# Performance work log

Measured on AMD Instinct MI355X. Metric: run time of the kernel, lower is better.

Reference implementation:

```python
import jax, jax.numpy as jnp
import numpy as np

N_NODES = 4096
N_GRAPHS = 32
N = N_NODES * N_GRAPHS          # 131072 total nodes
DEG = 32
E = N * DEG                      # 4194304 edges
IN_CH = 16
OUT_CH = 2
EPS_BN = 1e-5


def setup_inputs() -> dict:
    key = jax.random.key(0)
    ks = jax.random.split(key, 24)
    rn = lambda k, s, scale=0.1: (jax.random.normal(k, s, dtype=jnp.float32) * scale)
    return {
        "x": jax.random.normal(ks[0], (N, IN_CH), dtype=jnp.float32),
        "edge_index": jax.random.randint(ks[1], (2, E), 0, N),
        "edge_attr": jax.random.uniform(ks[2], (E, 3), dtype=jnp.float32),
        # GraphConv1: 16 -> 20  (lin_rel has bias, lin_root has no bias; PyG GraphConv)
        "W_rel1": rn(ks[3], (IN_CH, 20)), "b1": jnp.zeros((20,), jnp.float32), "W_root1": rn(ks[4], (IN_CH, 20)),
        # GraphConv2: 20 -> 20
        "W_rel2": rn(ks[5], (20, 20)), "b2": jnp.zeros((20,), jnp.float32), "W_root2": rn(ks[6], (20, 20)),
        # GraphConv3: 20 -> 1
        "W_rel3": rn(ks[7], (20, 1)), "b3": jnp.zeros((1,), jnp.float32), "W_root3": rn(ks[8], (20, 1)),
        # BatchNorm1d(num_nodes) affine params (channel dim = node index)
        "bn1_g": jnp.ones((N_NODES,), jnp.float32), "bn1_b": jnp.zeros((N_NODES,), jnp.float32),
        "bn2_g": jnp.ones((N_NODES,), jnp.float32), "bn2_b": jnp.zeros((N_NODES,), jnp.float32),
        # fc layers, stored [in, out]
        "fc1_W": rn(ks[9], (N_NODES, 50), 0.02), "fc1_b": jnp.zeros((50,), jnp.float32),
        "fc2_W": rn(ks[10], (50, OUT_CH)), "fc2_b": jnp.zeros((OUT_CH,), jnp.float32),
        "num_graphs": N_GRAPHS,
    }


def _graph_conv(x, src, dst, w, W_rel, b_rel, W_root):
    # PyG GraphConv: out_i = lin_root(x_i) + lin_rel( sum_{j->i} w_ji * x_j )
    msg = x[src] * w[:, None]                              # [E, F] gather + scale
    agg = jax.ops.segment_sum(msg, dst, num_segments=x.shape[0])  # scatter-add
    return agg @ W_rel + b_rel + x @ W_root


def _bn_nodes(h3, gamma, beta):
    # BatchNorm1d(num_nodes) in training mode: h3 is [B, num_nodes, F];
    # normalize per node-channel over (batch, feat), biased variance (torch training).
    mu = jnp.mean(h3, axis=(0, 2), keepdims=True)
    var = jnp.var(h3, axis=(0, 2), keepdims=True)
    hn = (h3 - mu) * jax.lax.rsqrt(var + EPS_BN)
    return hn * gamma[None, :, None] + beta[None, :, None]


def reference(x, edge_index, edge_attr,
              W_rel1, b1, W_root1, W_rel2, b2, W_root2, W_rel3, b3, W_root3,
              bn1_g, bn1_b, bn2_g, bn2_b, fc1_W, fc1_b, fc2_W, fc2_b, num_graphs):
    src, dst = edge_index[0], edge_index[1]
    w = edge_attr[:, 2]
    B = num_graphs

    h = _graph_conv(x, src, dst, w, W_rel1, b1, W_root1)
    h = jax.nn.leaky_relu(h)                                   # slope 0.01, matches torch default
    h = _bn_nodes(h.reshape(B, -1, h.shape[-1]), bn1_g, bn1_b).reshape(-1, h.shape[-1])

    h = _graph_conv(h, src, dst, w, W_rel2, b2, W_root2)
    h = jax.nn.leaky_relu(h)
    h = _bn_nodes(h.reshape(B, -1, h.shape[-1]), bn2_g, bn2_b).reshape(-1, h.shape[-1])

    h = _graph_conv(h, src, dst, w, W_rel3, b3, W_root3)
    h = jax.nn.leaky_relu(h)
    h = h.reshape(B, -1)                                        # [B, num_nodes]

    # per-graph normalization; note: divides by var (not std), var is unbiased (torch.var default)
    eps = 1e-10
    out = (h - jnp.mean(h, axis=1, keepdims=True)) / (jnp.var(h, axis=1, keepdims=True, ddof=1) + eps)
    out = jax.nn.leaky_relu(out @ fc1_W + fc1_b)
    # dropout omitted (eval-mode identity)
    out = out @ fc2_W + fc2_b
    return (out, h)
```

## Files before the change

### kernel.cpp

```cpp
#include <hip/hip_runtime.h>
#include <hip/hip_fp16.h>

#define N_NODES 4096
#define N_GRAPHS 32
#define NTOT (N_NODES * N_GRAPHS)
#define NE (NTOT * 32)
#define C1 16
#define C2 20
#define CAP 72

#define NBUCK 512
#define BSHIFT 8
#define BMASK 255
#define CAPB 8960
#define EPB1 8192

__device__ __forceinline__ float lrelu(float v) { return v > 0.f ? v : 0.01f * v; }

__device__ __forceinline__ unsigned pack_edge(int src, float w) {
    int k = __float2int_rn(w * 32768.f);
    if (k > 32767) k = 32767;
    return (unsigned)src | ((unsigned)k << 17);
}
__device__ __forceinline__ void unpack_edge(unsigned p, int& src, float& w) {
    src = (int)(p & 0x1FFFFu);
    w = (float)(p >> 17) * 3.0517578125e-5f;
}

__device__ __forceinline__ uint4 pack8h(const float* v) {
    union { uint4 u4; __half h[8]; } c;
#pragma unroll
    for (int q = 0; q < 8; q++) c.h[q] = __float2half(v[q]);
    return c.u4;
}
__device__ __forceinline__ uint2 pack4h(const float* v) {
    union { uint2 u2; __half h[4]; } c;
#pragma unroll
    for (int q = 0; q < 4; q++) c.h[q] = __float2half(v[q]);
    return c.u2;
}
__device__ __forceinline__ void fma8(uint4 u, float wv, float* acc) {
    union { uint4 u4; __half2 h2[4]; } c; c.u4 = u;
#pragma unroll
    for (int q = 0; q < 4; q++) {
        float2 f = __half22float2(c.h2[q]);
        acc[2 * q]     += f.x * wv;
        acc[2 * q + 1] += f.y * wv;
    }
}
__device__ __forceinline__ void fma4(uint2 u, float wv, float* acc) {
    union { uint2 u2; __half2 h2[2]; } c; c.u2 = u;
#pragma unroll
    for (int q = 0; q < 2; q++) {
        float2 f = __half22float2(c.h2[q]);
        acc[2 * q]     += f.x * wv;
        acc[2 * q + 1] += f.y * wv;
    }
}
__device__ __forceinline__ void unp8(uint4 u, float* v) {
    union { uint4 u4; __half2 h2[4]; } c; c.u4 = u;
#pragma unroll
    for (int q = 0; q < 4; q++) {
        float2 f = __half22float2(c.h2[q]);
        v[2 * q] = f.x; v[2 * q + 1] = f.y;
    }
}
__device__ __forceinline__ void unp4(uint2 u, float* v) {
    union { uint2 u2; __half2 h2[2]; } c; c.u2 = u;
#pragma unroll
    for (int q = 0; q < 2; q++) {
        float2 f = __half22float2(c.h2[q]);
        v[2 * q] = f.x; v[2 * q + 1] = f.y;
    }
}

__global__ __launch_bounds__(256) void k_part1(const int* __restrict__ ei,
                                               const float* __restrict__ ea,
                                               int* __restrict__ gcur,
                                               uint2* __restrict__ part) {
    __shared__ int hist[NBUCK];
    __shared__ int cur[NBUCK];
    int t = threadIdx.x;
    hist[t] = 0; hist[t + 256] = 0;
    __syncthreads();
    int base = blockIdx.x * EPB1;
#pragma unroll 4
    for (int i = 0; i < EPB1 / 256; i++) {
        int d = ei[NE + base + i * 256 + t];
        atomicAdd(&hist[d >> BSHIFT], 1);
    }
    __syncthreads();
    cur[t]       = atomicAdd(&gcur[t], hist[t]);
    cur[t + 256] = atomicAdd(&gcur[t + 256], hist[t + 256]);
    __syncthreads();
#pragma unroll 4
    for (int i = 0; i < EPB1 / 256; i++) {
        int e = base + i * 256 + t;
        int d = ei[NE + e];
        int b = d >> BSHIFT;
        int p = atomicAdd(&cur[b], 1);
        if (p < CAPB)
            part[(size_t)b * CAPB + p] = make_uint2(pack_edge(ei[e], ea[3 * e + 2]),
                                                    (unsigned)(d & BMASK));
    }
}

__global__ __launch_bounds__(256) void k_part2(const int* __restrict__ gcur,
                                               const uint2* __restrict__ part,
                                               unsigned* __restrict__ slots,
                                               int* __restrict__ cnt) {
    __shared__ int cur[256];
    int t = threadIdx.x;
    cur[t] = 0;
    __syncthreads();
    int b = blockIdx.x;
    int nrec = gcur[b]; if (nrec > CAPB) nrec = CAPB;
    const uint2* rp = part + (size_t)b * CAPB;
    int nb = b << BSHIFT;
    for (int i = t; i < nrec; i += 256) {
        uint2 r = rp[i];
        int ld = (int)r.y;
        int pos = atomicAdd(&cur[ld], 1);
        if (pos < CAP) slots[(size_t)pos * NTOT + nb + ld] = r.x;
    }
    __syncthreads();
    cnt[nb + t] = cur[t];
}

__global__ void k_fill_slots(const int* __restrict__ ei, const float* __restrict__ ea,
                             int* __restrict__ cnt, unsigned* __restrict__ slots) {
    int e = blockIdx.x * 256 + threadIdx.x;
    if (e >= NE) return;
    int d = ei[NE + e];
    int pos = atomicAdd(&cnt[d], 1);
    if (pos < CAP) slots[(size_t)pos * NTOT + d] = pack_edge(ei[e], ea[3 * e + 2]);
}

__global__ void k_xcast(const float* __restrict__ x, uint4* __restrict__ xa, uint4* __restrict__ xb) {
    int n = blockIdx.x * 256 + threadIdx.x;
    if (n >= NTOT) return;
    float xr[C1];
    const float4* xp = (const float4*)(x + (size_t)n * C1);
#pragma unroll
    for (int q = 0; q < 4; q++) ((float4*)xr)[q] = xp[q];
    xa[n] = pack8h(xr);
    xb[n] = pack8h(xr + 8);
}

__global__ __launch_bounds__(256) void k_conv1(const float* __restrict__ x,
                        const uint4* __restrict__ xa, const uint4* __restrict__ xb,
                        const unsigned* __restrict__ slots, const int* __restrict__ cnt,
                        const float* __restrict__ Wr, const float* __restrict__ bb,
                        const float* __restrict__ Wo, float* __restrict__ t1) {
    __shared__ float sWr[C1 * C2], sWo[C1 * C2], sb[C2];
    for (int k = threadIdx.x; k < C1 * C2; k += 256) { sWr[k] = Wr[k]; sWo[k] = Wo[k]; }
    if (threadIdx.x < C2) sb[threadIdx.x] = bb[threadIdx.x];
    __syncthreads();
    int n = blockIdx.x * 256 + threadIdx.x;
    int m = cnt[n]; if (m > CAP) m = CAP;
    float acc[C1];
#pragma unroll
    for (int i = 0; i < C1; i++) acc[i] = 0.f;
    {
        int i = 0;
        for (; i + 4 <= m; i += 4) {
            unsigned p0 = __builtin_nontemporal_load(slots + (size_t)(i + 0) * NTOT + n);
            unsigned p1 = __builtin_nontemporal_load(slots + (size_t)(i + 1) * NTOT + n);
            unsigned p2 = __builtin_nontemporal_load(slots + (size_t)(i + 2) * NTOT + n);
            unsigned p3 = __builtin_nontemporal_load(slots + (size_t)(i + 3) * NTOT + n);
            int s0, s1, s2, s3; float w0, w1, w2, w3;
            unpack_edge(p0, s0, w0); unpack_edge(p1, s1, w1);
            unpack_edge(p2, s2, w2); unpack_edge(p3, s3, w3);
            uint4 u0 = xa[s0], u1 = xa[s1], u2 = xa[s2], u3 = xa[s3];
            fma8(u0, w0, acc); fma8(u1, w1, acc); fma8(u2, w2, acc); fma8(u3, w3, acc);
        }
        for (; i < m; i++) {
            unsigned p = __builtin_nontemporal_load(slots + (size_t)i * NTOT + n);
            int s; float w; unpack_edge(p, s, w);
            fma8(xa[s], w, acc);
        }
    }
    {
        int i = 0;
        for (; i + 4 <= m; i += 4) {
            unsigned p0 = __builtin_nontemporal_load(slots + (size_t)(i + 0) * NTOT + n);
            unsigned p1 = __builtin_nontemporal_load(slots + (size_t)(i + 1) * NTOT + n);
            unsigned p2 = __builtin_nontemporal_load(slots + (size_t)(i + 2) * NTOT + n);
            unsigned p3 = __builtin_nontemporal_load(slots + (size_t)(i + 3) * NTOT + n);
            int s0, s1, s2, s3; float w0, w1, w2, w3;
            unpack_edge(p0, s0, w0); unpack_edge(p1, s1, w1);
            unpack_edge(p2, s2, w2); unpack_edge(p3, s3, w3);
            uint4 u0 = xb[s0], u1 = xb[s1], u2 = xb[s2], u3 = xb[s3];
            fma8(u0, w0, acc + 8); fma8(u1, w1, acc + 8); fma8(u2, w2, acc + 8); fma8(u3, w3, acc + 8);
        }
        for (; i < m; i++) {
            unsigned p = __builtin_nontemporal_load(slots + (size_t)i * NTOT + n);
            int s; float w; unpack_edge(p, s, w);
            fma8(xb[s], w, acc + 8);
        }
    }
    float xr[C1];
    const float4* xp = (const float4*)(x + (size_t)n * C1);
#pragma unroll
    for (int q = 0; q < 4; q++) ((float4*)xr)[q] = xp[q];
    float outv[C2];
#pragma unroll
    for (int j = 0; j < C2; j++) {
        float a = sb[j];
#pragma unroll
        for (int i = 0; i < C1; i++) a += acc[i] * sWr[i * C2 + j] + xr[i] * sWo[i * C2 + j];
        outv[j] = lrelu(a);
    }
    float4* op = (float4*)(t1 + (size_t)n * C2);
#pragma unroll
    for (int q = 0; q < 5; q++) op[q] = ((float4*)outv)[q];
}

__global__ void k_stats(const float* __restrict__ t, float* __restrict__ mu, float* __restrict__ rs) {
    int i = blockIdx.x;
    float s = 0.f, ss = 0.f;
    for (int k = threadIdx.x; k < N_GRAPHS * C2; k += 64) {
        int g = k / C2, j = k - g * C2;
        float v = t[((size_t)(g * N_NODES + i)) * C2 + j];
        s += v; ss += v * v;
    }
#pragma unroll
    for (int off = 32; off > 0; off >>= 1) { s += __shfl_down(s, off); ss += __shfl_down(ss, off); }
    if (threadIdx.x == 0) {
        float m = s * (1.f / (N_GRAPHS * C2));
        float var = ss * (1.f / (N_GRAPHS * C2)) - m * m;
        mu[i] = m;
        rs[i] = rsqrtf(var + 1e-5f);
    }
}

__global__ void k_bn_apply(const float* __restrict__ t, const float* __restrict__ mu,
                           const float* __restrict__ rs, const float* __restrict__ gam,
                           const float* __restrict__ bet, uint4* __restrict__ hnA,
                           uint2* __restrict__ hnB) {
    int n = blockIdx.x * 256 + threadIdx.x;
    if (n >= NTOT) return;
    int i = n & (N_NODES - 1);
    float sc = rs[i] * gam[i];
    float sh = bet[i] - mu[i] * sc;
    float v[C2];
    const float4* tp = (const float4*)(t + (size_t)n * C2);
#pragma unroll
    for (int q = 0; q < 5; q++) ((float4*)v)[q] = tp[q];
#pragma unroll
    for (int j = 0; j < C2; j++) v[j] = v[j] * sc + sh;
    hnA[n] = pack8h(v);
    uint2* hp = hnB + (size_t)n * 3;
    hp[0] = pack4h(v + 8);
    hp[1] = pack4h(v + 12);
    hp[2] = pack4h(v + 16);
}

__global__ __launch_bounds__(256) void k_conv2(const uint4* __restrict__ hnA,
                        const uint2* __restrict__ hnB,
                        const unsigned* __restrict__ slots, const int* __restrict__ cnt,
                        const float* __restrict__ Wr, const float* __restrict__ bb,
                        const float* __restrict__ Wo, float* __restrict__ t2) {
    __shared__ float sWr[C2 * C2], sWo[C2 * C2], sb[C2];
    for (int k = threadIdx.x; k < C2 * C2; k += 256) { sWr[k] = Wr[k]; sWo[k] = Wo[k]; }
    if (threadIdx.x < C2) sb[threadIdx.x] = bb[threadIdx.x];
    __syncthreads();
    int n = blockIdx.x * 256 + threadIdx.x;
    int m = cnt[n]; if (m > CAP) m = CAP;
    float acc[C2];
#pragma unroll
    for (int i = 0; i < C2; i++) acc[i] = 0.f;
    {
        int i = 0;
        for (; i + 4 <= m; i += 4) {
            unsigned p0 = __builtin_nontemporal_load(slots + (size_t)(i + 0) * NTOT + n);
            unsigned p1 = __builtin_nontemporal_load(slots + (size_t)(i + 1) * NTOT + n);
            unsigned p2 = __builtin_nontemporal_load(slots + (size_t)(i + 2) * NTOT + n);
            unsigned p3 = __builtin_nontemporal_load(slots + (size_t)(i + 3) * NTOT + n);
            int s0, s1, s2, s3; float w0, w1, w2, w3;
            unpack_edge(p0, s0, w0); unpack_edge(p1, s1, w1);
            unpack_edge(p2, s2, w2); unpack_edge(p3, s3, w3);
            uint4 u0 = hnA[s0], u1 = hnA[s1], u2 = hnA[s2], u3 = hnA[s3];
            fma8(u0, w0, acc); fma8(u1, w1, acc); fma8(u2, w2, acc); fma8(u3, w3, acc);
        }
        for (; i < m; i++) {
            unsigned p = __builtin_nontemporal_load(slots + (size_t)i * NTOT + n);
            int s; float w; unpack_edge(p, s, w);
            fma8(hnA[s], w, acc);
        }
    }
    {
        int i = 0;
        for (; i + 4 <= m; i += 4) {
            unsigned p0 = __builtin_nontemporal_load(slots + (size_t)(i + 0) * NTOT + n);
            unsigned p1 = __builtin_nontemporal_load(slots + (size_t)(i + 1) * NTOT + n);
            unsigned p2 = __builtin_nontemporal_load(slots + (size_t)(i + 2) * NTOT + n);
            unsigned p3 = __builtin_nontemporal_load(slots + (size_t)(i + 3) * NTOT + n);
            int s0, s1, s2, s3; float w0, w1, w2, w3;
            unpack_edge(p0, s0, w0); unpack_edge(p1, s1, w1);
            unpack_edge(p2, s2, w2); unpack_edge(p3, s3, w3);
            const uint2* r0 = hnB + (size_t)s0 * 3;
            const uint2* r1 = hnB + (size_t)s1 * 3;
            const uint2* r2 = hnB + (size_t)s2 * 3;
            const uint2* r3 = hnB + (size_t)s3 * 3;
            uint2 a0 = r0[0], b0 = r0[1], c0 = r0[2];
            uint2 a1 = r1[0], b1 = r1[1], c1 = r1[2];
            uint2 a2 = r2[0], b2 = r2[1], c2 = r2[2];
            uint2 a3 = r3[0], b3 = r3[1], c3 = r3[2];
            fma4(a0, w0, acc + 8); fma4(b0, w0, acc + 12); fma4(c0, w0, acc + 16);
            fma4(a1, w1, acc + 8); fma4(b1, w1, acc + 12); fma4(c1, w1, acc + 16);
            fma4(a2, w2, acc + 8); fma4(b2, w2, acc + 12); fma4(c2, w2, acc + 16);
            fma4(a3, w3, acc + 8); fma4(b3, w3, acc + 12); fma4(c3, w3, acc + 16);
        }
        for (; i < m; i++) {
            unsigned p = __builtin_nontemporal_load(slots + (size_t)i * NTOT + n);
            int s; float w; unpack_edge(p, s, w);
            const uint2* r = hnB + (size_t)s * 3;
            fma4(r[0], w, acc + 8); fma4(r[1], w, acc + 12); fma4(r[2], w, acc + 16);
        }
    }
    float h[C2];
    unp8(hnA[n], h);
    {
        const uint2* r = hnB + (size_t)n * 3;
        unp4(r[0], h + 8); unp4(r[1], h + 12); unp4(r[2], h + 16);
    }
    float outv[C2];
#pragma unroll
    for (int j = 0; j < C2; j++) {
        float a = sb[j];
#pragma unroll
        for (int i = 0; i < C2; i++) a += acc[i] * sWr[i * C2 + j] + h[i] * sWo[i * C2 + j];
        outv[j] = lrelu(a);
    }
    float4* op = (float4*)(t2 + (size_t)n * C2);
#pragma unroll
    for (int q = 0; q < 5; q++) op[q] = ((float4*)outv)[q];
}

__global__ void k_bn2_proj(const float* __restrict__ t, const float* __restrict__ mu,
                           const float* __restrict__ rs, const float* __restrict__ gam,
                           const float* __restrict__ bet, const float* __restrict__ Wr3,
                           const float* __restrict__ b3, const float* __restrict__ Wo3,
                           float* __restrict__ y, float* __restrict__ r2) {
    __shared__ float sWr[C2], sWo[C2];
    if (threadIdx.x < C2) { sWr[threadIdx.x] = Wr3[threadIdx.x]; sWo[threadIdx.x] = Wo3[threadIdx.x]; }
    __syncthreads();
    int n = blockIdx.x * 256 + threadIdx.x;
    if (n >= NTOT) return;
    int i = n & (N_NODES - 1);
    float sc = rs[i] * gam[i];
    float sh = bet[i] - mu[i] * sc;
    float v[C2];
    const float4* tp = (const float4*)(t + (size_t)n * C2);
#pragma unroll
    for (int q = 0; q < 5; q++) ((float4*)v)[q] = tp[q];
    float ay = 0.f, ar = 0.f;
#pragma unroll
    for (int j = 0; j < C2; j++) {
        float hv = v[j] * sc + sh;
        ay += hv * sWr[j];
        ar += hv * sWo[j];
    }
    y[n] = ay;
    r2[n] = ar + b3[0];
}

__global__ __launch_bounds__(256) void k_conv3(const float* __restrict__ y, const float* __restrict__ r2,
                        const unsigned* __restrict__ slots, const int* __restrict__ cnt,
                        float* __restrict__ hout, float* __restrict__ gsum, float* __restrict__ gss) {
    __shared__ float ls[4], lss[4];
    int n = blockIdx.x * 256 + threadIdx.x;
    int m = cnt[n]; if (m > CAP) m = CAP;
    float a = 0.f;
    int i = 0;
    for (; i + 4 <= m; i += 4) {
        unsigned p0 = __builtin_nontemporal_load(slots + (size_t)(i + 0) * NTOT + n);
        unsigned p1 = __builtin_nontemporal_load(slots + (size_t)(i + 1) * NTOT + n);
        unsigned p2 = __builtin_nontemporal_load(slots + (size_t)(i + 2) * NTOT + n);
        unsigned p3 = __builtin_nontemporal_load(slots + (size_t)(i + 3) * NTOT + n);
        int s0, s1, s2, s3; float w0, w1, w2, w3;
        unpack_edge(p0, s0, w0); unpack_edge(p1, s1, w1);
        unpack_edge(p2, s2, w2); unpack_edge(p3, s3, w3);
        a += y[s0] * w0 + y[s1] * w1 + y[s2] * w2 + y[s3] * w3;
    }
    for (; i < m; i++) {
        unsigned p = __builtin_nontemporal_load(slots + (size_t)i * NTOT + n);
        int s; float w; unpack_edge(p, s, w);
        a += y[s] * w;
    }
    float v = lrelu(a + r2[n]);
    hout[n] = v;
    float s = v, ss = v * v;
#pragma unroll
    for (int o = 32; o > 0; o >>= 1) { s += __shfl_down(s, o); ss += __shfl_down(ss, o); }
    int wid = threadIdx.x >> 6, lid = threadIdx.x & 63;
    if (lid == 0) { ls[wid] = s; lss[wid] = ss; }
    __syncthreads();
    if (threadIdx.x == 0) {
        int g = blockIdx.x >> 4;
        atomicAdd(&gsum[g], ls[0] + ls[1] + ls[2] + ls[3]);
        atomicAdd(&gss[g], lss[0] + lss[1] + lss[2] + lss[3]);
    }
}

__global__ void k_fc1(const float* __restrict__ h, const float* __restrict__ gsum,
                      const float* __restrict__ gss, const float* __restrict__ W,
                      const float* __restrict__ b, float* __restrict__ z) {
    __shared__ float ls[4];
    int blk = blockIdx.x;
    int g = blk / 50, k = blk - g * 50;
    float mu = gsum[g] / N_NODES;
    float var = (gss[g] - N_NODES * mu * mu) / (N_NODES - 1);
    float inv = 1.f / (var + 1e-10f);
    const float* hr = h + (size_t)g * N_NODES;
    float p = 0.f;
    for (int n = threadIdx.x; n < N_NODES; n += 256)
        p += (hr[n] - mu) * inv * W[(size_t)n * 50 + k];
#pragma unroll
    for (int off = 32; off > 0; off >>= 1) p += __shfl_down(p, off);
    int wid = threadIdx.x >> 6, lid = threadIdx.x & 63;
    if (lid == 0) ls[wid] = p;
    __syncthreads();
    if (threadIdx.x == 0) {
        float S = ls[0] + ls[1] + ls[2] + ls[3];
        z[g * 50 + k] = lrelu(S + b[k]);
    }
}

__global__ void k_fc2(const float* __restrict__ z, const float* __restrict__ W,
                      const float* __restrict__ b, float* __restrict__ out) {
    int t = threadIdx.x;
    if (t >= N_GRAPHS * 2) return;
    int g = t >> 1, o = t & 1;
    float acc = b[o];
#pragma unroll
    for (int k = 0; k < 50; k++) acc += z[g * 50 + k] * W[k * 2 + o];
    out[g * 2 + o] = acc;
}

extern "C" void kernel_launch(void* const* d_in, const int* in_sizes, int n_in,
                              void* d_out, int out_size, void* d_ws, size_t ws_size,
                              hipStream_t stream) {
    const float* x    = (const float*)d_in[0];
    const int*   ei   = (const int*)d_in[1];
    const float* ea   = (const float*)d_in[2];
    const float* Wr1  = (const float*)d_in[3];
    const float* b1   = (const float*)d_in[4];
    const float* Wo1  = (const float*)d_in[5];
    const float* Wr2  = (const float*)d_in[6];
    const float* b2   = (const float*)d_in[7];
    const float* Wo2  = (const float*)d_in[8];
    const float* Wr3  = (const float*)d_in[9];
    const float* b3   = (const float*)d_in[10];
    const float* Wo3  = (const float*)d_in[11];
    const float* bn1g = (const float*)d_in[12];
    const float* bn1b = (const float*)d_in[13];
    const float* bn2g = (const float*)d_in[14];
    const float* bn2b = (const float*)d_in[15];
    const float* fc1W = (const float*)d_in[16];
    const float* fc1b = (const float*)d_in[17];
    const float* fc2W = (const float*)d_in[18];
    const float* fc2b = (const float*)d_in[19];
    float* out = (float*)d_out;

    const size_t part_bytes  = (size_t)NBUCK * CAPB * sizeof(uint2);
    const size_t slots_bytes = (size_t)NTOT * CAP * sizeof(unsigned);
    const size_t tail_bytes  = (size_t)NTOT * C2 * sizeof(float)
                             + (size_t)NTOT * 16 * 3
                             + (size_t)NTOT * 24
                             + (size_t)NTOT * 2 * sizeof(float)
                             + (size_t)NTOT * sizeof(int)
                             + (size_t)(NBUCK + 4 * N_NODES + 8 * N_GRAPHS + N_GRAPHS * 50 + 64) * sizeof(float);
    const bool useSort = ws_size >= part_bytes + slots_bytes + tail_bytes;

    char* wsb = (char*)d_ws;
    uint2*    part  = (uint2*)wsb;     wsb += useSort ? part_bytes : 0;
    unsigned* slots = (unsigned*)wsb;  wsb += slots_bytes;
    float*    bufA  = (float*)wsb;     wsb += (size_t)NTOT * C2 * sizeof(float);
    uint4*    xa    = (uint4*)wsb;     wsb += (size_t)NTOT * 16;
    uint4*    xb    = (uint4*)wsb;     wsb += (size_t)NTOT * 16;
    uint4*    hnA   = (uint4*)wsb;     wsb += (size_t)NTOT * 16;
    uint2*    hnB   = (uint2*)wsb;     wsb += (size_t)NTOT * 24;
    float*    yv    = (float*)wsb;     wsb += (size_t)NTOT * sizeof(float);
    float*    r2v   = (float*)wsb;     wsb += (size_t)NTOT * sizeof(float);
    int*      cnt   = (int*)wsb;       wsb += (size_t)NTOT * sizeof(int);
    int*      gcur  = (int*)wsb;       wsb += NBUCK * sizeof(int);
    float*    mu1   = (float*)wsb;     wsb += N_NODES * sizeof(float);
    float*    rs1   = (float*)wsb;     wsb += N_NODES * sizeof(float);
    float*    mu2   = (float*)wsb;     wsb += N_NODES * sizeof(float);
    float*    rs2   = (float*)wsb;     wsb += N_NODES * sizeof(float);
    float*    gsum  = (float*)wsb;     wsb += N_GRAPHS * sizeof(float);
    float*    gss   = (float*)wsb;     wsb += N_GRAPHS * sizeof(float);
    float*    z     = (float*)wsb;     wsb += N_GRAPHS * 50 * sizeof(float);

    const int EB = (NE + 255) / 256;
    const int NB = (NTOT + 255) / 256;

    hipMemsetAsync(gsum, 0, 2 * N_GRAPHS * sizeof(float), stream);
    k_xcast<<<NB, 256, 0, stream>>>(x, xa, xb);
    if (useSort) {
        hipMemsetAsync(gcur, 0, NBUCK * sizeof(int), stream);
        k_part1<<<NE / EPB1, 256, 0, stream>>>(ei, ea, gcur, part);
        k_part2<<<NBUCK, 256, 0, stream>>>(gcur, part, slots, cnt);
    } else {
        hipMemsetAsync(cnt, 0, (size_t)NTOT * sizeof(int), stream);
        k_fill_slots<<<EB, 256, 0, stream>>>(ei, ea, cnt, slots);
    }

    k_conv1<<<NB, 256, 0, stream>>>(x, xa, xb, slots, cnt, Wr1, b1, Wo1, bufA);
    k_stats<<<N_NODES, 64, 0, stream>>>(bufA, mu1, rs1);
    k_bn_apply<<<NB, 256, 0, stream>>>(bufA, mu1, rs1, bn1g, bn1b, hnA, hnB);

    k_conv2<<<NB, 256, 0, stream>>>(hnA, hnB, slots, cnt, Wr2, b2, Wo2, bufA);
    k_stats<<<N_NODES, 64, 0, stream>>>(bufA, mu2, rs2);
    k_bn2_proj<<<NB, 256, 0, stream>>>(bufA, mu2, rs2, bn2g, bn2b, Wr3, b3, Wo3, yv, r2v);

    k_conv3<<<NB, 256, 0, stream>>>(yv, r2v, slots, cnt, out + 64, gsum, gss);

    k_fc1<<<N_GRAPHS * 50, 256, 0, stream>>>(out + 64, gsum, gss, fc1W, fc1b, z);
    k_fc2<<<1, 64, 0, stream>>>(z, fc2W, fc2b, out);
}
```

Before: 457.3 us.

## Split conv edge loops across wavefronts and stage partition writes in LDS

The three graph-conv kernels now assign several threads per node: the edge list is split in halves and the feature channels in groups across wavefronts, and partial sums are combined through shared memory before the dense projection, which is itself spread over four threads per node. This raises parallelism and memory-level concurrency for the gather-heavy aggregation, at the cost of extra LDS traffic, a barrier, and redundant slot loads. The bucket partition kernel now sorts records locally in LDS by bucket with a prefix scan and writes them out contiguously, so global writes coalesce instead of scattering per atomic slot. conv1 also reads root features from the fp16 copies rather than the fp32 input, which changes precision slightly.

```diff
diff --git a/kernel.cpp b/kernel.cpp
--- a/kernel.cpp
+++ b/kernel.cpp
@@ -78,30 +78,55 @@
                                                const float* __restrict__ ea,
                                                int* __restrict__ gcur,
                                                uint2* __restrict__ part) {
-    __shared__ int hist[NBUCK];
-    __shared__ int cur[NBUCK];
+    __shared__ unsigned lrecA[EPB1];
+    __shared__ unsigned char lrecB[EPB1];
+    __shared__ int hist[NBUCK], sscan[NBUCK], base[NBUCK], lcur[NBUCK];
+    __shared__ int ts[256];
     int t = threadIdx.x;
     hist[t] = 0; hist[t + 256] = 0;
     __syncthreads();
-    int base = blockIdx.x * EPB1;
-#pragma unroll 4
+    int eb = blockIdx.x * EPB1;
+    int dreg[EPB1 / 256];
+#pragma unroll
     for (int i = 0; i < EPB1 / 256; i++) {
-        int d = ei[NE + base + i * 256 + t];
+        int d = ei[NE + eb + i * 256 + t];
+        dreg[i] = d;
         atomicAdd(&hist[d >> BSHIFT], 1);
     }
     __syncthreads();
-    cur[t]       = atomicAdd(&gcur[t], hist[t]);
-    cur[t + 256] = atomicAdd(&gcur[t + 256], hist[t + 256]);
-    __syncthreads();
-#pragma unroll 4
+    int a0 = hist[2 * t], a1 = hist[2 * t + 1];
+    ts[t] = a0 + a1;
+    __syncthreads();
+    for (int d = 1; d < 256; d <<= 1) {
+        int v = (t >= d) ? ts[t - d] : 0;
+        __syncthreads();
+        ts[t] += v;
+        __syncthreads();
+    }
+    int excl = (t == 0) ? 0 : ts[t - 1];
+    sscan[2 * t] = excl;
+    sscan[2 * t + 1] = excl + a0;
+    lcur[2 * t] = excl;
+    lcur[2 * t + 1] = excl + a0;
+    base[t]       = atomicAdd(&gcur[t], hist[t]);
+    base[t + 256] = atomicAdd(&gcur[t + 256], hist[t + 256]);
+    __syncthreads();
+#pragma unroll
     for (int i = 0; i < EPB1 / 256; i++) {
-        int e = base + i * 256 + t;
-        int d = ei[NE + e];
+        int e = eb + i * 256 + t;
+        int d = dreg[i];
         int b = d >> BSHIFT;
-        int p = atomicAdd(&cur[b], 1);
-        if (p < CAPB)
-            part[(size_t)b * CAPB + p] = make_uint2(pack_edge(ei[e], ea[3 * e + 2]),
-                                                    (unsigned)(d & BMASK));
+        int pos = atomicAdd(&lcur[b], 1);
+        lrecA[pos] = pack_edge(ei[e], ea[3 * e + 2]);
+        lrecB[pos] = (unsigned char)(d & BMASK);
+    }
+    __syncthreads();
+    for (int j = t; j < EPB1; j += 256) {
+        int lo = 0, hi = NBUCK - 1;
+        while (lo < hi) { int mid = (lo + hi + 1) >> 1; if (sscan[mid] <= j) lo = mid; else hi = mid - 1; }
+        int b = lo;
+        int dp = base[b] + (j - sscan[b]);
+        if (dp < CAPB) part[(size_t)b * CAPB + dp] = make_uint2(lrecA[j], (unsigned)lrecB[j]);
     }
 }
 
@@ -147,73 +172,65 @@
     xb[n] = pack8h(xr + 8);
 }
 
-__global__ __launch_bounds__(256) void k_conv1(const float* __restrict__ x,
-                        const uint4* __restrict__ xa, const uint4* __restrict__ xb,
+__global__ __launch_bounds__(256) void k_conv1(const uint4* __restrict__ xa, const uint4* __restrict__ xb,
                         const unsigned* __restrict__ slots, const int* __restrict__ cnt,
                         const float* __restrict__ Wr, const float* __restrict__ bb,
                         const float* __restrict__ Wo, float* __restrict__ t1) {
     __shared__ float sWr[C1 * C2], sWo[C1 * C2], sb[C2];
+    __shared__ float sacc[4][64][8];
     for (int k = threadIdx.x; k < C1 * C2; k += 256) { sWr[k] = Wr[k]; sWo[k] = Wo[k]; }
     if (threadIdx.x < C2) sb[threadIdx.x] = bb[threadIdx.x];
-    __syncthreads();
-    int n = blockIdx.x * 256 + threadIdx.x;
-    int m = cnt[n]; if (m > CAP) m = CAP;
-    float acc[C1];
-#pragma unroll
-    for (int i = 0; i < C1; i++) acc[i] = 0.f;
-    {
-        int i = 0;
-        for (; i + 4 <= m; i += 4) {
-            unsigned p0 = __builtin_nontemporal_load(slots + (size_t)(i + 0) * NTOT + n);
-            unsigned p1 = __builtin_nontemporal_load(slots + (size_t)(i + 1) * NTOT + n);
-            unsigned p2 = __builtin_nontemporal_load(slots + (size_t)(i + 2) * NTOT + n);
-            unsigned p3 = __builtin_nontemporal_load(slots + (size_t)(i + 3) * NTOT + n);
-            int s0, s1, s2, s3; float w0, w1, w2, w3;
-            unpack_edge(p0, s0, w0); unpack_edge(p1, s1, w1);
-            unpack_edge(p2, s2, w2); unpack_edge(p3, s3, w3);
-            uint4 u0 = xa[s0], u1 = xa[s1], u2 = xa[s2], u3 = xa[s3];
-            fma8(u0, w0, acc); fma8(u1, w1, acc); fma8(u2, w2, acc); fma8(u3, w3, acc);
-        }
-        for (; i < m; i++) {
-            unsigned p = __builtin_nontemporal_load(slots + (size_t)i * NTOT + n);
-            int s; float w; unpack_edge(p, s, w);
-            fma8(xa[s], w, acc);
-        }
-    }
-    {
-        int i = 0;
-        for (; i + 4 <= m; i += 4) {
-            unsigned p0 = __builtin_nontemporal_load(slots + (size_t)(i + 0) * NTOT + n);
-            unsigned p1 = __builtin_nontemporal_load(slots + (size_t)(i + 1) * NTOT + n);
-            unsigned p2 = __builtin_nontemporal_load(slots + (size_t)(i + 2) * NTOT + n);
-            unsigned p3 = __builtin_nontemporal_load(slots + (size_t)(i + 3) * NTOT + n);
-            int s0, s1, s2, s3; float w0, w1, w2, w3;
-            unpack_edge(p0, s0, w0); unpack_edge(p1, s1, w1);
-            unpack_edge(p2, s2, w2); unpack_edge(p3, s3, w3);
-            uint4 u0 = xb[s0], u1 = xb[s1], u2 = xb[s2], u3 = xb[s3];
-            fma8(u0, w0, acc + 8); fma8(u1, w1, acc + 8); fma8(u2, w2, acc + 8); fma8(u3, w3, acc + 8);
-        }
-        for (; i < m; i++) {
-            unsigned p = __builtin_nontemporal_load(slots + (size_t)i * NTOT + n);
-            int s; float w; unpack_edge(p, s, w);
-            fma8(xb[s], w, acc + 8);
-        }
-    }
+    int nl = threadIdx.x & 63;
+    int sub = threadIdx.x >> 6;
+    int gn = blockIdx.x * 64 + nl;
+    int m = cnt[gn]; if (m > CAP) m = CAP;
+    int h0 = m >> 1;
+    int lo = (sub & 1) ? h0 : 0;
+    int hi = (sub & 1) ? m : h0;
+    const uint4* va = (sub < 2) ? xa : xb;
+    float acc[8];
+#pragma unroll
+    for (int q = 0; q < 8; q++) acc[q] = 0.f;
+    int i = lo;
+    for (; i + 4 <= hi; i += 4) {
+        unsigned p0 = __builtin_nontemporal_load(slots + (size_t)(i + 0) * NTOT + gn);
+        unsigned p1 = __builtin_nontemporal_load(slots + (size_t)(i + 1) * NTOT + gn);
+        unsigned p2 = __builtin_nontemporal_load(slots + (size_t)(i + 2) * NTOT + gn);
+        unsigned p3 = __builtin_nontemporal_load(slots + (size_t)(i + 3) * NTOT + gn);
+        int s0, s1, s2, s3; float w0, w1, w2, w3;
+        unpack_edge(p0, s0, w0); unpack_edge(p1, s1, w1);
+        unpack_edge(p2, s2, w2); unpack_edge(p3, s3, w3);
+        uint4 u0 = va[s0], u1 = va[s1], u2 = va[s2], u3 = va[s3];
+        fma8(u0, w0, acc); fma8(u1, w1, acc); fma8(u2, w2, acc); fma8(u3, w3, acc);
+    }
+    for (; i < hi; i++) {
+        unsigned p = __builtin_nontemporal_load(slots + (size_t)i * NTOT + gn);
+        int s; float w; unpack_edge(p, s, w);
+        fma8(va[s], w, acc);
+    }
+#pragma unroll
+    for (int q = 0; q < 8; q++) sacc[sub][nl][q] = acc[q];
+    __syncthreads();
+    int n2 = threadIdx.x >> 2, qq = threadIdx.x & 3;
+    int gn2 = blockIdx.x * 64 + n2;
+    float accf[C1];
+#pragma unroll
+    for (int q = 0; q < 8; q++) accf[q] = sacc[0][n2][q] + sacc[1][n2][q];
+#pragma unroll
+    for (int q = 0; q < 8; q++) accf[8 + q] = sacc[2][n2][q] + sacc[3][n2][q];
     float xr[C1];
-    const float4* xp = (const float4*)(x + (size_t)n * C1);
-#pragma unroll
-    for (int q = 0; q < 4; q++) ((float4*)xr)[q] = xp[q];
-    float outv[C2];
-#pragma unroll
-    for (int j = 0; j < C2; j++) {
+    unp8(xa[gn2], xr); unp8(xb[gn2], xr + 8);
+    float outv[5];
+#pragma unroll
+    for (int jj = 0; jj < 5; jj++) {
+        int j = qq * 5 + jj;
         float a = sb[j];
 #pragma unroll
-        for (int i = 0; i < C1; i++) a += acc[i] * sWr[i * C2 + j] + xr[i] * sWo[i * C2 + j];
-        outv[j] = lrelu(a);
-    }
-    float4* op = (float4*)(t1 + (size_t)n * C2);
-#pragma unroll
-    for (int q = 0; q < 5; q++) op[q] = ((float4*)outv)[q];
+        for (int q = 0; q < C1; q++) a += accf[q] * sWr[q * C2 + j] + xr[q] * sWo[q * C2 + j];
+        outv[jj] = lrelu(a);
+    }
+#pragma unroll
+    for (int jj = 0; jj < 5; jj++) t1[(size_t)gn2 * C2 + qq * 5 + jj] = outv[jj];
 }
 
 __global__ void k_stats(const float* __restrict__ t, float* __restrict__ mu, float* __restrict__ rs) {
@@ -262,40 +279,50 @@
                         const float* __restrict__ Wr, const float* __restrict__ bb,
                         const float* __restrict__ Wo, float* __restrict__ t2) {
     __shared__ float sWr[C2 * C2], sWo[C2 * C2], sb[C2];
+    __shared__ float saccA[2][64][8];
+    __shared__ float saccB[2][64][12];
     for (int k = threadIdx.x; k < C2 * C2; k += 256) { sWr[k] = Wr[k]; sWo[k] = Wo[k]; }
     if (threadIdx.x < C2) sb[threadIdx.x] = bb[threadIdx.x];
-    __syncthreads();
-    int n = blockIdx.x * 256 + threadIdx.x;
-    int m = cnt[n]; if (m > CAP) m = CAP;
-    float acc[C2];
-#pragma unroll
-    for (int i = 0; i < C2; i++) acc[i] = 0.f;
-    {
-        int i = 0;
-        for (; i + 4 <= m; i += 4) {
-            unsigned p0 = __builtin_nontemporal_load(slots + (size_t)(i + 0) * NTOT + n);
-            unsigned p1 = __builtin_nontemporal_load(slots + (size_t)(i + 1) * NTOT + n);
-            unsigned p2 = __builtin_nontemporal_load(slots + (size_t)(i + 2) * NTOT + n);
-            unsigned p3 = __builtin_nontemporal_load(slots + (size_t)(i + 3) * NTOT + n);
+    int nl = threadIdx.x & 63;
+    int sub = threadIdx.x >> 6;
+    int gn = blockIdx.x * 64 + nl;
+    int m = cnt[gn]; if (m > CAP) m = CAP;
+    int h0 = m >> 1;
+    int lo = (sub & 1) ? h0 : 0;
+    int hi = (sub & 1) ? m : h0;
+    if (sub < 2) {
+        float acc[8];
+#pragma unroll
+        for (int q = 0; q < 8; q++) acc[q] = 0.f;
+        int i = lo;
+        for (; i + 4 <= hi; i += 4) {
+            unsigned p0 = __builtin_nontemporal_load(slots + (size_t)(i + 0) * NTOT + gn);
+            unsigned p1 = __builtin_nontemporal_load(slots + (size_t)(i + 1) * NTOT + gn);
+            unsigned p2 = __builtin_nontemporal_load(slots + (size_t)(i + 2) * NTOT + gn);
+            unsigned p3 = __builtin_nontemporal_load(slots + (size_t)(i + 3) * NTOT + gn);
             int s0, s1, s2, s3; float w0, w1, w2, w3;
             unpack_edge(p0, s0, w0); unpack_edge(p1, s1, w1);
             unpack_edge(p2, s2, w2); unpack_edge(p3, s3, w3);
             uint4 u0 = hnA[s0], u1 = hnA[s1], u2 = hnA[s2], u3 = hnA[s3];
             fma8(u0, w0, acc); fma8(u1, w1, acc); fma8(u2, w2, acc); fma8(u3, w3, acc);
         }
-        for (; i < m; i++) {
-            unsigned p = __builtin_nontemporal_load(slots + (size_t)i * NTOT + n);
+        for (; i < hi; i++) {
+            unsigned p = __builtin_nontemporal_load(slots + (size_t)i * NTOT + gn);
             int s; float w; unpack_edge(p, s, w);
             fma8(hnA[s], w, acc);
         }
-    }
-    {
-        int i = 0;
-        for (; i + 4 <= m; i += 4) {
-            unsigned p0 = __builtin_nontemporal_load(slots + (size_t)(i + 0) * NTOT + n);
-            unsigned p1 = __builtin_nontemporal_load(slots + (size_t)(i + 1) * NTOT + n);
-            unsigned p2 = __builtin_nontemporal_load(slots + (size_t)(i + 2) * NTOT + n);
-            unsigned p3 = __builtin_nontemporal_load(slots + (size_t)(i + 3) * NTOT + n);
+#pragma unroll
+        for (int q = 0; q < 8; q++) saccA[sub][nl][q] = acc[q];
+    } else {
+        float acc[12];
+#pragma unroll
+        for (int q = 0; q < 12; q++) acc[q] = 0.f;
+        int i = lo;
+        for (; i + 4 <= hi; i += 4) {
+            unsigned p0 = __builtin_nontemporal_load(slots + (size_t)(i + 0) * NTOT + gn);
+            unsigned p1 = __builtin_nontemporal_load(slots + (size_t)(i + 1) * NTOT + gn);
+            unsigned p2 = __builtin_nontemporal_load(slots + (size_t)(i + 2) * NTOT + gn);
+            unsigned p3 = __builtin_nontemporal_load(slots + (size_t)(i + 3) * NTOT + gn);
             int s0, s1, s2, s3; float w0, w1, w2, w3;
             unpack_edge(p0, s0, w0); unpack_edge(p1, s1, w1);
             unpack_edge(p2, s2, w2); unpack_edge(p3, s3, w3);
@@ -307,35 +334,45 @@
             uint2 a1 = r1[0], b1 = r1[1], c1 = r1[2];
             uint2 a2 = r2[0], b2 = r2[1], c2 = r2[2];
             uint2 a3 = r3[0], b3 = r3[1], c3 = r3[2];
-            fma4(a0, w0, acc + 8); fma4(b0, w0, acc + 12); fma4(c0, w0, acc + 16);
-            fma4(a1, w1, acc + 8); fma4(b1, w1, acc + 12); fma4(c1, w1, acc + 16);
-            fma4(a2, w2, acc + 8); fma4(b2, w2, acc + 12); fma4(c2, w2, acc + 16);
-            fma4(a3, w3, acc + 8); fma4(b3, w3, acc + 12); fma4(c3, w3, acc + 16);
+            fma4(a0, w0, acc); fma4(b0, w0, acc + 4); fma4(c0, w0, acc + 8);
+            fma4(a1, w1, acc); fma4(b1, w1, acc + 4); fma4(c1, w1, acc + 8);
+            fma4(a2, w2, acc); fma4(b2, w2, acc + 4); fma4(c2, w2, acc + 8);
+            fma4(a3, w3, acc); fma4(b3, w3, acc + 4); fma4(c3, w3, acc + 8);
         }
-        for (; i < m; i++) {
-            unsigned p = __builtin_nontemporal_load(slots + (size_t)i * NTOT + n);
+        for (; i < hi; i++) {
+            unsigned p = __builtin_nontemporal_load(slots + (size_t)i * NTOT + gn);
             int s; float w; unpack_edge(p, s, w);
             const uint2* r = hnB + (size_t)s * 3;
-            fma4(r[0], w, acc + 8); fma4(r[1], w, acc + 12); fma4(r[2], w, acc + 16);
+            fma4(r[0], w, acc); fma4(r[1], w, acc + 4); fma4(r[2], w, acc + 8);
         }
-    }
+#pragma unroll
+        for (int q = 0; q < 12; q++) saccB[sub - 2][nl][q] = acc[q];
+    }
+    __syncthreads();
+    int n2 = threadIdx.x >> 2, qq = threadIdx.x & 3;
+    int gn2 = blockIdx.x * 64 + n2;
+    float accf[C2];
+#pragma unroll
+    for (int q = 0; q < 8; q++) accf[q] = saccA[0][n2][q] + saccA[1][n2][q];
+#pragma unroll
+    for (int q = 0; q < 12; q++) accf[8 + q] = saccB[0][n2][q] + saccB[1][n2][q];
     float h[C2];
-    unp8(hnA[n], h);
+    unp8(hnA[gn2], h);
     {
-        const uint2* r = hnB + (size_t)n * 3;
+        const uint2* r = hnB + (size_t)gn2 * 3;
         unp4(r[0], h + 8); unp4(r[1], h + 12); unp4(r[2], h + 16);
     }
-    float outv[C2];
-#pragma unroll
-    for (int j = 0; j < C2; j++) {
+    float outv[5];
+#pragma unroll
+    for (int jj = 0; jj < 5; jj++) {
+        int j = qq * 5 + jj;
         float a = sb[j];
 #pragma unroll
-        for (int i = 0; i < C2; i++) a += acc[i] * sWr[i * C2 + j] + h[i] * sWo[i * C2 + j];
-        outv[j] = lrelu(a);
-    }
-    float4* op = (float4*)(t2 + (size_t)n * C2);
-#pragma unroll
-    for (int q = 0; q < 5; q++) op[q] = ((float4*)outv)[q];
+        for (int q = 0; q < C2; q++) a += accf[q] * sWr[q * C2 + j] + h[q] * sWo[q * C2 + j];
+        outv[jj] = lrelu(a);
+    }
+#pragma unroll
+    for (int jj = 0; jj < 5; jj++) t2[(size_t)gn2 * C2 + qq * 5 + jj] = outv[jj];
 }
 
 __global__ void k_bn2_proj(const float* __restrict__ t, const float* __restrict__ mu,
@@ -369,12 +406,18 @@
 __global__ __launch_bounds__(256) void k_conv3(const float* __restrict__ y, const float* __restrict__ r2,
                         const unsigned* __restrict__ slots, const int* __restrict__ cnt,
                         float* __restrict__ hout, float* __restrict__ gsum, float* __restrict__ gss) {
+    __shared__ float pbuf[2][128];
     __shared__ float ls[4], lss[4];
-    int n = blockIdx.x * 256 + threadIdx.x;
+    int nl = threadIdx.x & 127;
+    int half = threadIdx.x >> 7;
+    int n = blockIdx.x * 128 + nl;
     int m = cnt[n]; if (m > CAP) m = CAP;
+    int h0 = m >> 1;
+    int lo = half ? h0 : 0;
+    int hi = half ? m : h0;
     float a = 0.f;
-    int i = 0;
-    for (; i + 4 <= m; i += 4) {
+    int i = lo;
+    for (; i + 4 <= hi; i += 4) {
         unsigned p0 = __builtin_nontemporal_load(slots + (size_t)(i + 0) * NTOT + n);
         unsigned p1 = __builtin_nontemporal_load(slots + (size_t)(i + 1) * NTOT + n);
         unsigned p2 = __builtin_nontemporal_load(slots + (size_t)(i + 2) * NTOT + n);
@@ -384,13 +427,18 @@
         unpack_edge(p2, s2, w2); unpack_edge(p3, s3, w3);
         a += y[s0] * w0 + y[s1] * w1 + y[s2] * w2 + y[s3] * w3;
     }
-    for (; i < m; i++) {
+    for (; i < hi; i++) {
         unsigned p = __builtin_nontemporal_load(slots + (size_t)i * NTOT + n);
         int s; float w; unpack_edge(p, s, w);
         a += y[s] * w;
     }
-    float v = lrelu(a + r2[n]);
-    hout[n] = v;
+    pbuf[half][nl] = a;
+    __syncthreads();
+    float v = 0.f;
+    if (half == 0) {
+        v = lrelu(pbuf[0][nl] + pbuf[1][nl] + r2[n]);
+        hout[n] = v;
+    }
     float s = v, ss = v * v;
 #pragma unroll
     for (int o = 32; o > 0; o >>= 1) { s += __shfl_down(s, o); ss += __shfl_down(ss, o); }
@@ -398,7 +446,7 @@
     if (lid == 0) { ls[wid] = s; lss[wid] = ss; }
     __syncthreads();
     if (threadIdx.x == 0) {
-        int g = blockIdx.x >> 4;
+        int g = blockIdx.x >> 5;
         atomicAdd(&gsum[g], ls[0] + ls[1] + ls[2] + ls[3]);
         atomicAdd(&gss[g], lss[0] + lss[1] + lss[2] + lss[3]);
     }
@@ -508,15 +556,15 @@
         k_fill_slots<<<EB, 256, 0, stream>>>(ei, ea, cnt, slots);
     }
 
-    k_conv1<<<NB, 256, 0, stream>>>(x, xa, xb, slots, cnt, Wr1, b1, Wo1, bufA);
+    k_conv1<<<NTOT / 64, 256, 0, stream>>>(xa, xb, slots, cnt, Wr1, b1, Wo1, bufA);
     k_stats<<<N_NODES, 64, 0, stream>>>(bufA, mu1, rs1);
     k_bn_apply<<<NB, 256, 0, stream>>>(bufA, mu1, rs1, bn1g, bn1b, hnA, hnB);
 
-    k_conv2<<<NB, 256, 0, stream>>>(hnA, hnB, slots, cnt, Wr2, b2, Wo2, bufA);
+    k_conv2<<<NTOT / 64, 256, 0, stream>>>(hnA, hnB, slots, cnt, Wr2, b2, Wo2, bufA);
     k_stats<<<N_NODES, 64, 0, stream>>>(bufA, mu2, rs2);
     k_bn2_proj<<<NB, 256, 0, stream>>>(bufA, mu2, rs2, bn2g, bn2b, Wr3, b3, Wo3, yv, r2v);
 
-    k_conv3<<<NB, 256, 0, stream>>>(yv, r2v, slots, cnt, out + 64, gsum, gss);
+    k_conv3<<<NTOT / 128, 256, 0, stream>>>(yv, r2v, slots, cnt, out + 64, gsum, gss);
 
     k_fc1<<<N_GRAPHS * 50, 256, 0, stream>>>(out + 64, gsum, gss, fc1W, fc1b, z);
     k_fc2<<<1, 64, 0, stream>>>(z, fc2W, fc2b, out);
```

New measurement: 488.9 us. 1.07x slower.

## Stage partition writes in shared memory for coalesced global stores

Applied to the files above, without the earlier changes.

k_part1 now does a local counting sort of each block's edges in LDS: it scans the bucket histogram and then writes contiguous runs to each bucket's partition, instead of scattering random 8-byte stores. k_part2 is split into two blocks per bucket, each handling 128 destination nodes. Each block builds a slot tile in shared memory and writes slot rows out coalesced rather than storing one strided element at a time. This trades extra shared memory (about 41KB per k_part1 block and 37KB per k_part2 block), a binary search per record, and each k_part2 block reading its whole bucket twice over, for far less uncoalesced global write traffic.

```diff
diff --git a/kernel.cpp b/kernel.cpp
--- a/kernel.cpp
+++ b/kernel.cpp
@@ -78,30 +78,55 @@
                                                const float* __restrict__ ea,
                                                int* __restrict__ gcur,
                                                uint2* __restrict__ part) {
-    __shared__ int hist[NBUCK];
-    __shared__ int cur[NBUCK];
+    __shared__ unsigned lrecA[EPB1];
+    __shared__ unsigned char lrecB[EPB1];
+    __shared__ int hist[NBUCK], sscan[NBUCK], base[NBUCK], lcur[NBUCK];
+    __shared__ int ts[256];
     int t = threadIdx.x;
     hist[t] = 0; hist[t + 256] = 0;
     __syncthreads();
-    int base = blockIdx.x * EPB1;
-#pragma unroll 4
+    int eb = blockIdx.x * EPB1;
+    int dreg[EPB1 / 256];
+#pragma unroll
     for (int i = 0; i < EPB1 / 256; i++) {
-        int d = ei[NE + base + i * 256 + t];
+        int d = ei[NE + eb + i * 256 + t];
+        dreg[i] = d;
         atomicAdd(&hist[d >> BSHIFT], 1);
     }
     __syncthreads();
-    cur[t]       = atomicAdd(&gcur[t], hist[t]);
-    cur[t + 256] = atomicAdd(&gcur[t + 256], hist[t + 256]);
-    __syncthreads();
-#pragma unroll 4
+    int a0 = hist[2 * t], a1 = hist[2 * t + 1];
+    ts[t] = a0 + a1;
+    __syncthreads();
+    for (int d = 1; d < 256; d <<= 1) {
+        int v = (t >= d) ? ts[t - d] : 0;
+        __syncthreads();
+        ts[t] += v;
+        __syncthreads();
+    }
+    int excl = (t == 0) ? 0 : ts[t - 1];
+    sscan[2 * t] = excl;
+    sscan[2 * t + 1] = excl + a0;
+    lcur[2 * t] = excl;
+    lcur[2 * t + 1] = excl + a0;
+    base[t]       = atomicAdd(&gcur[t], hist[t]);
+    base[t + 256] = atomicAdd(&gcur[t + 256], hist[t + 256]);
+    __syncthreads();
+#pragma unroll
     for (int i = 0; i < EPB1 / 256; i++) {
-        int e = base + i * 256 + t;
-        int d = ei[NE + e];
+        int e = eb + i * 256 + t;
+        int d = dreg[i];
         int b = d >> BSHIFT;
-        int p = atomicAdd(&cur[b], 1);
-        if (p < CAPB)
-            part[(size_t)b * CAPB + p] = make_uint2(pack_edge(ei[e], ea[3 * e + 2]),
-                                                    (unsigned)(d & BMASK));
+        int pos = atomicAdd(&lcur[b], 1);
+        lrecA[pos] = pack_edge(ei[e], ea[3 * e + 2]);
+        lrecB[pos] = (unsigned char)(d & BMASK);
+    }
+    __syncthreads();
+    for (int j = t; j < EPB1; j += 256) {
+        int lo = 0, hi = NBUCK - 1;
+        while (lo < hi) { int mid = (lo + hi + 1) >> 1; if (sscan[mid] <= j) lo = mid; else hi = mid - 1; }
+        int b = lo;
+        int dp = base[b] + (j - sscan[b]);
+        if (dp < CAPB) part[(size_t)b * CAPB + dp] = make_uint2(lrecA[j], (unsigned)lrecB[j]);
     }
 }
 
@@ -109,22 +134,35 @@
                                                const uint2* __restrict__ part,
                                                unsigned* __restrict__ slots,
                                                int* __restrict__ cnt) {
-    __shared__ int cur[256];
+    __shared__ unsigned tile[128 * CAP];
+    __shared__ int cur[128];
+    __shared__ int maxc;
     int t = threadIdx.x;
-    cur[t] = 0;
-    __syncthreads();
-    int b = blockIdx.x;
+    if (t < 128) cur[t] = 0;
+    if (t == 0) maxc = 0;
+    __syncthreads();
+    int b = blockIdx.x >> 1;
+    int halfsel = blockIdx.x & 1;
+    int nbase = (b << BSHIFT) + (halfsel << 7);
     int nrec = gcur[b]; if (nrec > CAPB) nrec = CAPB;
     const uint2* rp = part + (size_t)b * CAPB;
-    int nb = b << BSHIFT;
     for (int i = t; i < nrec; i += 256) {
         uint2 r = rp[i];
         int ld = (int)r.y;
-        int pos = atomicAdd(&cur[ld], 1);
-        if (pos < CAP) slots[(size_t)pos * NTOT + nb + ld] = r.x;
-    }
-    __syncthreads();
-    cnt[nb + t] = cur[t];
+        if ((ld >> 7) == halfsel) {
+            int l = ld & 127;
+            int pos = atomicAdd(&cur[l], 1);
+            if (pos < CAP) tile[pos * 128 + l] = r.x;
+        }
+    }
+    __syncthreads();
+    if (t < 128) { cnt[nbase + t] = cur[t]; atomicMax(&maxc, cur[t]); }
+    __syncthreads();
+    int mc = maxc; if (mc > CAP) mc = CAP;
+    for (int j = t; j < mc * 128; j += 256) {
+        int pos = j >> 7, l = j & 127;
+        slots[(size_t)pos * NTOT + nbase + l] = tile[j];
+    }
 }
 
 __global__ void k_fill_slots(const int* __restrict__ ei, const float* __restrict__ ea,
@@ -502,7 +540,7 @@
     if (useSort) {
         hipMemsetAsync(gcur, 0, NBUCK * sizeof(int), stream);
         k_part1<<<NE / EPB1, 256, 0, stream>>>(ei, ea, gcur, part);
-        k_part2<<<NBUCK, 256, 0, stream>>>(gcur, part, slots, cnt);
+        k_part2<<<NBUCK * 2, 256, 0, stream>>>(gcur, part, slots, cnt);
     } else {
         hipMemsetAsync(cnt, 0, (size_t)NTOT * sizeof(int), stream);
         k_fill_slots<<<EB, 256, 0, stream>>>(ei, ea, cnt, slots);
```

Result: faster. 433.1 us (-5.3%).
